# Performance work log

Hardware: AMD Instinct MI355X
Metric: run time of the kernel (lower is better)

Reference implementation:

```python
import jax, jax.numpy as jnp
import numpy as np

R = 40000      # aug_num_rels
E = 500000     # number of relation-graph triplets
DIN = 64       # rel_emb_dim
DH = 64        # hid_dim_rel
H = 8          # num_head
DHID = DH // H # 8
NBIN = 10
L = 2          # num_layer_rel


def _leaky(x):
    return jax.nn.leaky_relu(x, negative_slope=0.2)


def _rel_layer(emb_rel, head, tail, binidx, pw, pb, abin, avec, aw, ab):
    # emb_rel: [R, DH]; head/tail/binidx: [E]
    concat = jnp.concatenate([emb_rel[head], emb_rel[tail]], axis=-1)  # [E, 2*DH]
    z = _leaky(concat @ pw + pb).reshape(-1, H, DHID)                   # [E, H, DHID]
    # attention logits: per-head dot with attn_vec + leaky(bin bias)
    raw = (z * avec[None]).sum(-1) + _leaky(abin[binidx, :, 0])         # [E, H]
    # segmented softmax over edges grouped by head index
    m = jax.ops.segment_max(raw, head, num_segments=R)                  # [R, H]
    e = jnp.exp(raw - m[head])                                          # [E, H]
    s = jax.ops.segment_sum(e, head, num_segments=R)                    # [R, H]
    beta = e / (s[head] + 1e-16)                                        # [E, H]
    msg = (emb_rel[tail] @ aw + ab).reshape(-1, H, DHID) * beta[..., None]
    out = jax.ops.segment_sum(msg, head, num_segments=R)                # [R, H, DHID]
    return out.reshape(R, DH)


def setup_inputs() -> dict:
    key = jax.random.key(0)
    ks = jax.random.split(key, 12)
    ht = jax.random.randint(ks[0], (E, 2), 0, R)
    b = jax.random.randint(ks[1], (E, 1), 0, NBIN)
    relation_triplets = jnp.concatenate([ht, b], axis=-1).astype(jnp.int64)
    sc = 0.05
    return {
        "relation_triplets": relation_triplets,
        "rel_emb_w": jax.random.normal(ks[2], (R, DIN), jnp.float32) * sc,
        "proj1_w": jax.random.normal(ks[3], (DIN, DH), jnp.float32) * sc,
        "proj1_b": jnp.zeros((DH,), jnp.float32),
        "attn_proj_w": jax.random.normal(ks[4], (L, 2 * DH, DH), jnp.float32) * sc,
        "attn_proj_b": jnp.zeros((L, DH), jnp.float32),
        "attn_bin": jax.random.normal(ks[5], (L, NBIN, H, 1), jnp.float32) * sc,
        "attn_vec": jax.random.normal(ks[6], (L, H, DHID), jnp.float32) * sc,
        "aggr_w": jax.random.normal(ks[7], (L, DH, DH), jnp.float32) * sc,
        "aggr_b": jnp.zeros((L, DH), jnp.float32),
        "res_w": jax.random.normal(ks[8], (L, DH, DH), jnp.float32) * sc,
        "res_b": jnp.zeros((L, DH), jnp.float32),
    }


def reference(relation_triplets, rel_emb_w, proj1_w, proj1_b, attn_proj_w,
              attn_proj_b, attn_bin, attn_vec, aggr_w, aggr_b, res_w, res_b):
    head = relation_triplets[:, 0]
    tail = relation_triplets[:, 1]
    binidx = relation_triplets[:, 2]
    emb_rel = jax.nn.relu(rel_emb_w @ proj1_w + proj1_b)  # [R, DH]
    for l in range(L):
        h = _rel_layer(emb_rel, head, tail, binidx,
                       attn_proj_w[l], attn_proj_b[l], attn_bin[l],
                       attn_vec[l], aggr_w[l], aggr_b[l])
        h = jax.nn.relu(h)
        emb_rel = h + jax.nn.relu(emb_rel @ res_w[l] + res_b[l])
    return emb_rel
```

## Files before the change

### kernel.cpp

```cpp
#include <hip/hip_runtime.h>
#include <hip/hip_bf16.h>

typedef __hip_bfloat16 bf16;

#define R_NUM 40000
#define E_NUM 500000
#define HIST_BLOCKS 1954
#define XF_BLOCKS 1250

#define N_CNTS 0
#define N_ROWP 160000
#define N_STB 320000
#define N_XMP0 2320384
#define N_HR0 12560384
#define N_XMP1 33040384
#define N_HR1 43280384
#define NEED2 63760384ull

#define W_P1W 0
#define W_P1B 4096
#define W_APW 4160
#define W_APB 20544
#define W_ABIN 20672
#define W_AVEC 20832
#define W_AW 20960
#define W_AB 29152
#define W_RW 29280
#define W_RB 37472
#define W_END 37600
#define WCONV_BLOCKS 147

#define O_FLAG 0
#define O_WBUF 256
#define O_ROWP 150784
#define O_CNTS 310784
#define O_TMP 470784
#define O_PART 634624
#define O_STB 635136
#define O_BIG 2635392

static __device__ __forceinline__ float b2f(bf16 x) { return __bfloat162float(x); }
static __device__ __forceinline__ float ldv(const float* p, size_t i) { return p[i]; }
static __device__ __forceinline__ float ldv(const bf16* p, size_t i) { return __bfloat162float(p[i]); }
static __device__ __forceinline__ void stv(float* p, size_t i, float v) { p[i] = v; }
static __device__ __forceinline__ void stv(bf16* p, size_t i, float v) { p[i] = __float2bfloat16(v); }

static __device__ __forceinline__ unsigned int f2bb(float x) {
  union { float f; unsigned int u; } v;
  v.f = x;
  unsigned int r = v.u + 0x7FFFu + ((v.u >> 16) & 1u);
  return r >> 16;
}
static __device__ __forceinline__ unsigned int packxm(float xt, float mt) {
  return f2bb(xt) | (f2bb(mt) << 16);
}

static __device__ __forceinline__ void load_edge(const unsigned int* __restrict__ w, int e,
                                                 int i64, int& h, int& t, int& b) {
  if (i64) {
    h = (int)w[6 * e + 0];
    t = (int)w[6 * e + 2];
    b = (int)w[6 * e + 4];
  } else {
    h = (int)w[3 * e + 0];
    t = (int)w[3 * e + 1];
    b = (int)w[3 * e + 2];
  }
}


__global__ void k_detect_init(const unsigned int* __restrict__ trip_w,
                              const unsigned short* __restrict__ emb_w, int* __restrict__ flag,
                              int* __restrict__ counts, int* __restrict__ stb) {
  int tid = threadIdx.x;
  if (blockIdx.x == 0) {
    if (tid < 64) {
      int lane = tid;
      unsigned int acc = 0;
      for (int i = lane; i < 1024; i += 64) acc |= trip_w[2 * i + 1];
      int votes = 0;
      for (int i = lane; i < 2048; i += 64) {
        unsigned short u = emb_w[2 * i];
        int ex = (u >> 7) & 0xFF;
        if (ex >= 90 && ex <= 130) votes++;
      }
      for (int off = 1; off < 64; off <<= 1) {
        acc |= __shfl_xor(acc, off);
        votes += __shfl_xor(votes, off);
      }
      if (lane == 0) {
        flag[0] = (acc == 0) ? 1 : 0;
        flag[1] = (votes < 1024) ? 1 : 0;
      }
    }
    return;
  }
  int g = (blockIdx.x - 1) * 256 + tid;
  for (int i = g; i < R_NUM; i += 159 * 256) counts[i] = 0;
  if (blockIdx.x == 1 && tid < 64) stb[E_NUM + tid] = 0;
}


template <typename WT>
static __device__ __forceinline__ void xf4t(const float (*sA)[64], int base, int j, int l,
                                            const WT* __restrict__ apw, const WT* __restrict__ apb,
                                            const WT* __restrict__ aw, const WT* __restrict__ ab,
                                            const WT* __restrict__ rw, const WT* __restrict__ rb,
                                            int r0, unsigned int* __restrict__ XMp,
                                            float2* __restrict__ HR) {
  const WT* pwt = apw + l * 8192;
  const WT* pwb = pwt + 4096;
  const WT* awl = aw + l * 4096;
  const WT* rwl = rw + l * 4096;
  float axt[8] = {0.f, 0.f, 0.f, 0.f, 0.f, 0.f, 0.f, 0.f};
  float amt[8] = {0.f, 0.f, 0.f, 0.f, 0.f, 0.f, 0.f, 0.f};
  float axh[8] = {0.f, 0.f, 0.f, 0.f, 0.f, 0.f, 0.f, 0.f};
  float ars[8] = {0.f, 0.f, 0.f, 0.f, 0.f, 0.f, 0.f, 0.f};
  for (int i4 = 0; i4 < 64; i4 += 4) {
    float4 ev[8];
#pragma unroll
    for (int n = 0; n < 8; n++) ev[n] = *(const float4*)&sA[base + n][i4];
#pragma unroll
    for (int di = 0; di < 4; di++) {
      int i = i4 + di;
      float wt = ldv(pwb, (size_t)i * 64 + j);
      float wm = ldv(awl, (size_t)i * 64 + j);
      float wh = ldv(pwt, (size_t)i * 64 + j);
      float wr = ldv(rwl, (size_t)i * 64 + j);
#pragma unroll
      for (int n = 0; n < 8; n++) {
        float e = ((const float*)&ev[n])[di];
        axt[n] = fmaf(e, wt, axt[n]);
        amt[n] = fmaf(e, wm, amt[n]);
        axh[n] = fmaf(e, wh, axh[n]);
        ars[n] = fmaf(e, wr, ars[n]);
      }
    }
  }
  float abj = ldv(ab, (size_t)l * 64 + j);
  float pbj = ldv(apb, (size_t)l * 64 + j);
  float rbj = ldv(rb, (size_t)l * 64 + j);
#pragma unroll
  for (int n = 0; n < 8; n++) {
    XMp[(size_t)(r0 + n) * 64 + j] = packxm(axt[n], amt[n] + abj);
    HR[(size_t)(r0 + n) * 64 + j] = make_float2(axh[n] + pbj, fmaxf(ars[n] + rbj, 0.f));
  }
}


template <typename T>
static __device__ __forceinline__ void kA_xform(const T* __restrict__ A, const T* __restrict__ p1w,
                                                const T* __restrict__ p1b,
                                                const T* __restrict__ apw,
                                                const T* __restrict__ apb, const T* __restrict__ aw,
                                                const T* __restrict__ ab, const T* __restrict__ rw,
                                                const T* __restrict__ rb, int u,
                                                unsigned int* __restrict__ XMp0,
                                                float2* __restrict__ HR0, float (*sA)[64]) {
  int tid = threadIdx.x;
  int j = tid & 63;
  int g = tid >> 6;
  int base = g * 8;
  for (int k = tid; k < 2048; k += 256) {
    int rr = k >> 6, cc = k & 63;
    sA[rr][cc] = ldv(A, (size_t)(u * 32 + rr) * 64 + cc);
  }
  __syncthreads();
  float a[8] = {0.f, 0.f, 0.f, 0.f, 0.f, 0.f, 0.f, 0.f};
  for (int i4 = 0; i4 < 64; i4 += 4) {
    float4 ev[8];
#pragma unroll
    for (int n = 0; n < 8; n++) ev[n] = *(const float4*)&sA[base + n][i4];
#pragma unroll
    for (int di = 0; di < 4; di++) {
      float w = ldv(p1w, (size_t)(i4 + di) * 64 + j);
#pragma unroll
      for (int n = 0; n < 8; n++) a[n] = fmaf(((const float*)&ev[n])[di], w, a[n]);
    }
  }
  float bj = ldv(p1b, j);
#pragma unroll
  for (int n = 0; n < 8; n++) a[n] = fmaxf(a[n] + bj, 0.f);
  __syncthreads();
#pragma unroll
  for (int n = 0; n < 8; n++) sA[base + n][j] = a[n];
  __syncthreads();
  xf4t<T>((const float(*)[64])sA, base, j, 0, apw, apb, aw, ab, rw, rb, u * 32 + base, XMp0, HR0);
}

__global__ void __launch_bounds__(256, 4) kA(const unsigned int* __restrict__ trip_w,
                                             const int* __restrict__ flag,
                                             const void* __restrict__ A, const void* p1w,
                                             const void* p1b, const void* apw, const void* apb,
                                             const void* aw, const void* ab, const void* rw,
                                             const void* rb, int* __restrict__ counts,
                                             unsigned int* __restrict__ XMp0,
                                             float2* __restrict__ HR0) {
  if (blockIdx.x < HIST_BLOCKS) {
    int e = blockIdx.x * 256 + threadIdx.x;
    if (e < E_NUM) {
      int h = flag[0] ? (int)trip_w[6 * e] : (int)trip_w[3 * e];
      atomicAdd(&counts[h], 1);
    }
    return;
  }
  __shared__ float sA[32][64];
  int u = blockIdx.x - HIST_BLOCKS;
  if (flag[1])
    kA_xform<float>((const float*)A, (const float*)p1w, (const float*)p1b, (const float*)apw,
                    (const float*)apb, (const float*)aw, (const float*)ab, (const float*)rw,
                    (const float*)rb, u, XMp0, HR0, sA);
  else
    kA_xform<bf16>((const bf16*)A, (const bf16*)p1w, (const bf16*)p1b, (const bf16*)apw,
                   (const bf16*)apb, (const bf16*)aw, (const bf16*)ab, (const bf16*)rw,
                   (const bf16*)rb, u, XMp0, HR0, sA);
}


__global__ void __launch_bounds__(1024) k_scan1(const int* __restrict__ counts,
                                                int* __restrict__ row_ptr) {
  __shared__ int sp[1024];
  int tid = threadIdx.x;
  int base = tid * 40;
  int local[40];
  int s = 0;
  if (base < R_NUM) {
#pragma unroll
    for (int k = 0; k < 40; k++) {
      int v = counts[base + k];
      local[k] = s;
      s += v;
    }
  }
  sp[tid] = s;
  __syncthreads();
  for (int off = 1; off < 1024; off <<= 1) {
    int t = (tid >= off) ? sp[tid - off] : 0;
    __syncthreads();
    sp[tid] += t;
    __syncthreads();
  }
  int pre = (tid == 0) ? 0 : sp[tid - 1];
  if (base < R_NUM) {
#pragma unroll
    for (int k = 0; k < 40; k++) row_ptr[base + k] = pre + local[k];
  }
}

__global__ void k_scatter(const unsigned int* __restrict__ trip_w, const int* __restrict__ flag,
                          int* __restrict__ row_ptr, int* __restrict__ stb) {
  int e = blockIdx.x * 256 + threadIdx.x;
  if (e >= E_NUM) return;
  int h, t, b;
  load_edge(trip_w, e, flag[0], h, t, b);
  int pos = atomicAdd(&row_ptr[h], 1);
  stb[pos] = (t & 0xFFFF) | (b << 16);
}


template <typename T>
static __device__ __forceinline__ void kB_body(const int* __restrict__ row_ptr,
                                               const int* __restrict__ stb,
                                               const unsigned int* __restrict__ XMp0,
                                               const float2* __restrict__ HR0,
                                               const T* __restrict__ apw, const T* __restrict__ apb,
                                               const T* __restrict__ abin,
                                               const T* __restrict__ avec, const T* __restrict__ aw,
                                               const T* __restrict__ ab, const T* __restrict__ rw,
                                               const T* __restrict__ rb,
                                               unsigned int* __restrict__ XMp1,
                                               float2* __restrict__ HR1, float (*sE)[64],
                                               float* sab) {
  int tid = threadIdx.x;
  int lane = tid & 63;
  int w = tid >> 6;
  int hh = lane >> 3;
  if (tid < 80) {
    float a = ldv(abin, tid);
    sab[tid] = (a > 0.f) ? a : 0.2f * a;
  }
  __syncthreads();
  float av = ldv(avec, lane);
  int rbase = blockIdx.x * 32 + w * 8;
#pragma unroll 1
  for (int n = 0; n < 8; n++) {
    int r = rbase + n;
    float2 hr = HR0[(size_t)r * 64 + lane];
    int beg = (r == 0) ? 0 : row_ptr[r - 1];
    int end = row_ptr[r];
    beg = __builtin_amdgcn_readfirstlane(beg);
    end = __builtin_amdgcn_readfirstlane(end);
    float xh = hr.x;
    float num = 0.f, den = 0.f;
    for (int jj = beg; jj < end; jj += 16) {
      int pk[16];
      unsigned int xp[16];
#pragma unroll
      for (int k = 0; k < 16; k++) pk[k] = stb[jj + k];
#pragma unroll
      for (int k = 0; k < 16; k++) xp[k] = XMp0[(size_t)(pk[k] & 0xFFFF) * 64 + lane];
#pragma unroll
      for (int k = 0; k < 16; k++) {
        float xt = __uint_as_float(xp[k] << 16);
        float mt = __uint_as_float(xp[k] & 0xFFFF0000u);
        float z = xh + xt;
        z = (z > 0.f) ? z : 0.2f * z;
        float v = z * av;
        v += __shfl_xor(v, 1);
        v += __shfl_xor(v, 2);
        v += __shfl_xor(v, 4);
        float e = __expf(v + sab[(pk[k] >> 16) * 8 + hh]);
        e = (jj + k < end) ? e : 0.f;
        den += e;
        num = fmaf(mt, e, num);
      }
    }
    sE[w * 8 + n][lane] = fmaxf(num / (den + 1e-16f), 0.f) + hr.y;
  }
  __syncthreads();
  xf4t<T>((const float(*)[64])sE, w * 8, lane, 1, apw, apb, aw, ab, rw, rb,
          blockIdx.x * 32 + w * 8, XMp1, HR1);
}

__global__ void __launch_bounds__(256, 4) kB(const int* __restrict__ row_ptr,
                                             const int* __restrict__ stb,
                                             const int* __restrict__ flag,
                                             const unsigned int* __restrict__ XMp0,
                                             const float2* __restrict__ HR0, const void* apw,
                                             const void* apb, const void* abin, const void* avec,
                                             const void* aw, const void* ab, const void* rw,
                                             const void* rb, unsigned int* __restrict__ XMp1,
                                             float2* __restrict__ HR1) {
  __shared__ float sE[32][64];
  __shared__ float sab[80];
  if (flag[1])
    kB_body<float>(row_ptr, stb, XMp0, HR0, (const float*)apw, (const float*)apb,
                   (const float*)abin, (const float*)avec, (const float*)aw, (const float*)ab,
                   (const float*)rw, (const float*)rb, XMp1, HR1, sE, sab);
  else
    kB_body<bf16>(row_ptr, stb, XMp0, HR0, (const bf16*)apw, (const bf16*)apb, (const bf16*)abin,
                  (const bf16*)avec, (const bf16*)aw, (const bf16*)ab, (const bf16*)rw,
                  (const bf16*)rb, XMp1, HR1, sE, sab);
}


template <typename T>
static __device__ __forceinline__ void kC_body(const int* __restrict__ row_ptr,
                                               const int* __restrict__ stb,
                                               const unsigned int* __restrict__ XMp1,
                                               const float2* __restrict__ HR1,
                                               const T* __restrict__ abin,
                                               const T* __restrict__ avec,
                                               float* __restrict__ out, float* sab) {
  int tid = threadIdx.x;
  int lane = tid & 63;
  int w = tid >> 6;
  int hh = lane >> 3;
  if (tid < 80) {
    float a = ldv(abin, 80 + tid);
    sab[tid] = (a > 0.f) ? a : 0.2f * a;
  }
  __syncthreads();
  float av = ldv(avec, 64 + lane);

  int r = blockIdx.x * 4 + w;
  float2 hr = HR1[(size_t)r * 64 + lane];
  int beg = (r == 0) ? 0 : row_ptr[r - 1];
  int end = row_ptr[r];
  beg = __builtin_amdgcn_readfirstlane(beg);
  end = __builtin_amdgcn_readfirstlane(end);

  float xh = hr.x;
  float num = 0.f, den = 0.f;
  for (int j = beg; j < end; j += 16) {
    int pk[16];
    unsigned int xp[16];
#pragma unroll
    for (int k = 0; k < 16; k++) pk[k] = stb[j + k];
#pragma unroll
    for (int k = 0; k < 16; k++) xp[k] = XMp1[(size_t)(pk[k] & 0xFFFF) * 64 + lane];
#pragma unroll
    for (int k = 0; k < 16; k++) {
      float xt = __uint_as_float(xp[k] << 16);
      float mt = __uint_as_float(xp[k] & 0xFFFF0000u);
      float z = xh + xt;
      z = (z > 0.f) ? z : 0.2f * z;
      float v = z * av;
      v += __shfl_xor(v, 1);
      v += __shfl_xor(v, 2);
      v += __shfl_xor(v, 4);
      float e = __expf(v + sab[(pk[k] >> 16) * 8 + hh]);
      e = (j + k < end) ? e : 0.f;
      den += e;
      num = fmaf(mt, e, num);
    }
  }
  out[(size_t)r * 64 + lane] = fmaxf(num / (den + 1e-16f), 0.f) + hr.y;
}

__global__ void __launch_bounds__(256, 4) kC(const int* __restrict__ row_ptr,
                                             const int* __restrict__ stb,
                                             const int* __restrict__ flag,
                                             const unsigned int* __restrict__ XMp1,
                                             const float2* __restrict__ HR1, const void* abin,
                                             const void* avec, float* __restrict__ out) {
  __shared__ float sab[80];
  if (flag[1])
    kC_body<float>(row_ptr, stb, XMp1, HR1, (const float*)abin, (const float*)avec, out, sab);
  else
    kC_body<bf16>(row_ptr, stb, XMp1, HR1, (const bf16*)abin, (const bf16*)avec, out, sab);
}


__global__ void k_hist_wconv(const unsigned int* __restrict__ trip_w, const int* __restrict__ flag,
                             int* __restrict__ counts, const void* p1w, const void* p1b,
                             const void* apw, const void* apb, const void* abin, const void* avec,
                             const void* aw, const void* ab, const void* rw, const void* rb,
                             float* __restrict__ wbuf) {
  if (blockIdx.x < WCONV_BLOCKS) {
    int i = blockIdx.x * 256 + threadIdx.x;
    if (i >= W_END) return;
    const void* src;
    int off;
    if (i < W_P1B) { src = p1w; off = i - W_P1W; }
    else if (i < W_APW) { src = p1b; off = i - W_P1B; }
    else if (i < W_APB) { src = apw; off = i - W_APW; }
    else if (i < W_ABIN) { src = apb; off = i - W_APB; }
    else if (i < W_AVEC) { src = abin; off = i - W_ABIN; }
    else if (i < W_AW) { src = avec; off = i - W_AVEC; }
    else if (i < W_AB) { src = aw; off = i - W_AW; }
    else if (i < W_RW) { src = ab; off = i - W_AB; }
    else if (i < W_RB) { src = rw; off = i - W_RW; }
    else { src = rb; off = i - W_RB; }
    wbuf[i] = flag[1] ? ((const float*)src)[off] : b2f(((const bf16*)src)[off]);
    return;
  }
  int e = (blockIdx.x - WCONV_BLOCKS) * 256 + threadIdx.x;
  if (e >= E_NUM) return;
  int h, t, b;
  load_edge(trip_w, e, flag[0], h, t, b);
  atomicAdd(&counts[h], 1);
}

__global__ void k_emb0(const void* __restrict__ A, const int* __restrict__ flag,
                       const float* __restrict__ wbuf, float* __restrict__ emb) {
  int j = threadIdx.x & 63;
  int g = threadIdx.x >> 6;
  int r0 = blockIdx.x * 16 + g * 4;
  int f32 = flag[1];
  __shared__ float sA[16][64];
  for (int k = threadIdx.x; k < 1024; k += 256) {
    int rr = k >> 6, cc = k & 63;
    size_t idx = (size_t)(blockIdx.x * 16 + rr) * 64 + cc;
    sA[rr][cc] = f32 ? ((const float*)A)[idx] : b2f(((const bf16*)A)[idx]);
  }
  __syncthreads();
  const float* W = wbuf + W_P1W;
  float a[4] = {0.f, 0.f, 0.f, 0.f};
  int base = g * 4;
  for (int i = 0; i < 64; i++) {
    float w = W[i * 64 + j];
#pragma unroll
    for (int n = 0; n < 4; n++) a[n] = fmaf(sA[base + n][i], w, a[n]);
  }
  float bj = wbuf[W_P1B + j];
#pragma unroll
  for (int n = 0; n < 4; n++)
    emb[(size_t)(r0 + n) * 64 + j] = fmaxf(a[n] + bj, 0.f);
}

static __device__ __forceinline__ float dotcol(const float* __restrict__ Wm, float val, int lane) {
  float acc = 0.f;
  for (int i = 0; i < 64; i++) acc = fmaf(__shfl(val, i), Wm[i * 64 + lane], acc);
  return acc;
}

template <typename TIN, typename TOUT>
__global__ void k_edge_d(const int* __restrict__ row_ptr, const int* __restrict__ stb,
                         const float* __restrict__ wbuf, int l, const TIN* __restrict__ emb_in,
                         TOUT* __restrict__ emb_out) {
  __shared__ float sab[80];
  int tid = threadIdx.x;
  int lane = tid & 63;
  int w = tid >> 6;
  int r = blockIdx.x * 4 + w;
  int hh = lane >> 3;
  if (tid < 80) {
    float a = wbuf[W_ABIN + l * 80 + tid];
    sab[tid] = (a > 0.f) ? a : 0.2f * a;
  }
  __syncthreads();
  const float* pwt = wbuf + W_APW + l * 8192;
  const float* pwb = pwt + 4096;
  const float* aw = wbuf + W_AW + l * 4096;
  const float* rw = wbuf + W_RW + l * 4096;

  float ev = ldv(emb_in, (size_t)r * 64 + lane);
  float xh = wbuf[W_APB + l * 64 + lane];
  float res = wbuf[W_RB + l * 64 + lane];
  for (int i = 0; i < 64; i++) {
    float e = __shfl(ev, i);
    xh = fmaf(e, pwt[i * 64 + lane], xh);
    res = fmaf(e, rw[i * 64 + lane], res);
  }
  res = fmaxf(res, 0.f);
  float av = wbuf[W_AVEC + l * 64 + lane];
  float abl = wbuf[W_AB + l * 64 + lane];

  int beg = (r == 0) ? 0 : row_ptr[r - 1];
  int end = row_ptr[r];
  float num = 0.f, den = 0.f;
  for (int j = beg; j < end; j++) {
    int p = stb[j];
    int t = p & 0xFFFF;
    float tv = ldv(emb_in, (size_t)t * 64 + lane);
    float z = xh + dotcol(pwb, tv, lane);
    z = (z > 0.f) ? z : 0.2f * z;
    float v = z * av;
    v += __shfl_xor(v, 1);
    v += __shfl_xor(v, 2);
    v += __shfl_xor(v, 4);
    float e = __expf(v + sab[(p >> 16) * 8 + hh]);
    den += e;
    float mt = dotcol(aw, tv, lane) + abl;
    num = fmaf(mt, e, num);
  }
  stv(emb_out, (size_t)r * 64 + lane, fmaxf(num / (den + 1e-16f), 0.f) + res);
}


extern "C" void kernel_launch(void* const* d_in, const int* in_sizes, int n_in,
                              void* d_out, int out_size, void* d_ws, size_t ws_size,
                              hipStream_t stream) {
  const unsigned int* trip_w = (const unsigned int*)d_in[0];
  const void* rel_emb = d_in[1];
  float* emb = (float*)d_out;
  char* ws = (char*)d_ws;

  if (ws_size >= NEED2) {
    int* counts = (int*)(ws + N_CNTS);
    int* row_ptr = (int*)(ws + N_ROWP);
    int* stb = (int*)(ws + N_STB);
    unsigned int* XMp0 = (unsigned int*)(ws + N_XMP0);
    float2* HR0 = (float2*)(ws + N_HR0);
    unsigned int* XMp1 = (unsigned int*)(ws + N_XMP1);
    float2* HR1 = (float2*)(ws + N_HR1);
    int* flag = (int*)(ws + N_STB + (E_NUM + 64) * 4);

    k_detect_init<<<160, 256, 0, stream>>>(trip_w, (const unsigned short*)rel_emb, flag, counts,
                                           stb);
    kA<<<HIST_BLOCKS + XF_BLOCKS, 256, 0, stream>>>(trip_w, flag, rel_emb, d_in[2], d_in[3],
                                                    d_in[4], d_in[5], d_in[8], d_in[9], d_in[10],
                                                    d_in[11], counts, XMp0, HR0);
    k_scan1<<<1, 1024, 0, stream>>>(counts, row_ptr);
    k_scatter<<<HIST_BLOCKS, 256, 0, stream>>>(trip_w, flag, row_ptr, stb);
    kB<<<XF_BLOCKS, 256, 0, stream>>>(row_ptr, stb, flag, XMp0, HR0, d_in[4], d_in[5], d_in[6],
                                      d_in[7], d_in[8], d_in[9], d_in[10], d_in[11], XMp1, HR1);
    kC<<<R_NUM / 4, 256, 0, stream>>>(row_ptr, stb, flag, XMp1, HR1, d_in[6], d_in[7], emb);
    return;
  }

  {
    int* flag = (int*)(ws + O_FLAG);
    float* wbuf = (float*)(ws + O_WBUF);
    int* row_ptr = (int*)(ws + O_ROWP);
    int* counts = (int*)(ws + O_CNTS);
    int* stb = (int*)(ws + O_STB);
    char* big = ws + O_BIG;

    k_detect_init<<<160, 256, 0, stream>>>(trip_w, (const unsigned short*)rel_emb, flag, counts,
                                           stb);
    k_hist_wconv<<<WCONV_BLOCKS + HIST_BLOCKS, 256, 0, stream>>>(
        trip_w, flag, counts, d_in[2], d_in[3], d_in[4], d_in[5], d_in[6], d_in[7], d_in[8],
        d_in[9], d_in[10], d_in[11], wbuf);
    k_scan1<<<1, 1024, 0, stream>>>(counts, row_ptr);
    k_scatter<<<HIST_BLOCKS, 256, 0, stream>>>(trip_w, flag, row_ptr, stb);
    k_emb0<<<R_NUM / 16, 256, 0, stream>>>(rel_emb, flag, wbuf, emb);
    bf16* embB = (bf16*)big;
    k_edge_d<float, bf16><<<R_NUM / 4, 256, 0, stream>>>(row_ptr, stb, wbuf, 0, emb, embB);
    k_edge_d<bf16, float><<<R_NUM / 4, 256, 0, stream>>>(row_ptr, stb, wbuf, 1, embB, emb);
  }
}
```

Measured before the change: 267.5 us.

## Use one wave per relation in layer-1 aggregation and fuse transform via shuffles

The layer-1 aggregation kernel now assigns one wavefront per relation row (10000 blocks of 4 waves) instead of 8 rows per wave in 1250 blocks. The following 64x64 transforms are computed per row by broadcasting the aggregated value across lanes with shuffles, which removes the shared staging buffer and block barrier. The goal is more parallelism and better load balance over uneven segment lengths. In exchange, weights are re-read per row with no reuse across rows, and the transform does more shuffles. The kA grid is also reordered so transform blocks launch before histogram blocks.

```diff
diff --git a/kernel.cpp b/kernel.cpp
--- a/kernel.cpp
+++ b/kernel.cpp
@@ -6,7 +6,7 @@
 #define R_NUM 40000
 #define E_NUM 500000
 #define HIST_BLOCKS 1954
-#define XF_BLOCKS 1250
+#define XFA_BLOCKS 1250
 
 #define N_CNTS 0
 #define N_ROWP 160000
@@ -101,7 +101,7 @@
 }
 
 
-template <typename WT>
+template <typename WT, int N>
 static __device__ __forceinline__ void xf4t(const float (*sA)[64], int base, int j, int l,
                                             const WT* __restrict__ apw, const WT* __restrict__ apb,
                                             const WT* __restrict__ aw, const WT* __restrict__ ab,
@@ -112,14 +112,14 @@
   const WT* pwb = pwt + 4096;
   const WT* awl = aw + l * 4096;
   const WT* rwl = rw + l * 4096;
-  float axt[8] = {0.f, 0.f, 0.f, 0.f, 0.f, 0.f, 0.f, 0.f};
-  float amt[8] = {0.f, 0.f, 0.f, 0.f, 0.f, 0.f, 0.f, 0.f};
-  float axh[8] = {0.f, 0.f, 0.f, 0.f, 0.f, 0.f, 0.f, 0.f};
-  float ars[8] = {0.f, 0.f, 0.f, 0.f, 0.f, 0.f, 0.f, 0.f};
+  float axt[N] = {};
+  float amt[N] = {};
+  float axh[N] = {};
+  float ars[N] = {};
   for (int i4 = 0; i4 < 64; i4 += 4) {
-    float4 ev[8];
-#pragma unroll
-    for (int n = 0; n < 8; n++) ev[n] = *(const float4*)&sA[base + n][i4];
+    float4 ev[N];
+#pragma unroll
+    for (int n = 0; n < N; n++) ev[n] = *(const float4*)&sA[base + n][i4];
 #pragma unroll
     for (int di = 0; di < 4; di++) {
       int i = i4 + di;
@@ -128,7 +128,7 @@
       float wh = ldv(pwt, (size_t)i * 64 + j);
       float wr = ldv(rwl, (size_t)i * 64 + j);
 #pragma unroll
-      for (int n = 0; n < 8; n++) {
+      for (int n = 0; n < N; n++) {
         float e = ((const float*)&ev[n])[di];
         axt[n] = fmaf(e, wt, axt[n]);
         amt[n] = fmaf(e, wm, amt[n]);
@@ -141,7 +141,7 @@
   float pbj = ldv(apb, (size_t)l * 64 + j);
   float rbj = ldv(rb, (size_t)l * 64 + j);
 #pragma unroll
-  for (int n = 0; n < 8; n++) {
+  for (int n = 0; n < N; n++) {
     XMp[(size_t)(r0 + n) * 64 + j] = packxm(axt[n], amt[n] + abj);
     HR[(size_t)(r0 + n) * 64 + j] = make_float2(axh[n] + pbj, fmaxf(ars[n] + rbj, 0.f));
   }
@@ -173,9 +173,9 @@
     for (int n = 0; n < 8; n++) ev[n] = *(const float4*)&sA[base + n][i4];
 #pragma unroll
     for (int di = 0; di < 4; di++) {
-      float w = ldv(p1w, (size_t)(i4 + di) * 64 + j);
-#pragma unroll
-      for (int n = 0; n < 8; n++) a[n] = fmaf(((const float*)&ev[n])[di], w, a[n]);
+      float wv = ldv(p1w, (size_t)(i4 + di) * 64 + j);
+#pragma unroll
+      for (int n = 0; n < 8; n++) a[n] = fmaf(((const float*)&ev[n])[di], wv, a[n]);
     }
   }
   float bj = ldv(p1b, j);
@@ -185,7 +185,8 @@
 #pragma unroll
   for (int n = 0; n < 8; n++) sA[base + n][j] = a[n];
   __syncthreads();
-  xf4t<T>((const float(*)[64])sA, base, j, 0, apw, apb, aw, ab, rw, rb, u * 32 + base, XMp0, HR0);
+  xf4t<T, 8>((const float(*)[64])sA, base, j, 0, apw, apb, aw, ab, rw, rb, u * 32 + base, XMp0,
+             HR0);
 }
 
 __global__ void __launch_bounds__(256, 4) kA(const unsigned int* __restrict__ trip_w,
@@ -196,8 +197,8 @@
                                              const void* rb, int* __restrict__ counts,
                                              unsigned int* __restrict__ XMp0,
                                              float2* __restrict__ HR0) {
-  if (blockIdx.x < HIST_BLOCKS) {
-    int e = blockIdx.x * 256 + threadIdx.x;
+  if (blockIdx.x >= XFA_BLOCKS) {
+    int e = (blockIdx.x - XFA_BLOCKS) * 256 + threadIdx.x;
     if (e < E_NUM) {
       int h = flag[0] ? (int)trip_w[6 * e] : (int)trip_w[3 * e];
       atomicAdd(&counts[h], 1);
@@ -205,7 +206,7 @@
     return;
   }
   __shared__ float sA[32][64];
-  int u = blockIdx.x - HIST_BLOCKS;
+  int u = blockIdx.x;
   if (flag[1])
     kA_xform<float>((const float*)A, (const float*)p1w, (const float*)p1b, (const float*)apw,
                     (const float*)apb, (const float*)aw, (const float*)ab, (const float*)rw,
@@ -259,18 +260,18 @@
 
 
 template <typename T>
-static __device__ __forceinline__ void kB_body(const int* __restrict__ row_ptr,
-                                               const int* __restrict__ stb,
-                                               const unsigned int* __restrict__ XMp0,
-                                               const float2* __restrict__ HR0,
-                                               const T* __restrict__ apw, const T* __restrict__ apb,
-                                               const T* __restrict__ abin,
-                                               const T* __restrict__ avec, const T* __restrict__ aw,
-                                               const T* __restrict__ ab, const T* __restrict__ rw,
-                                               const T* __restrict__ rb,
-                                               unsigned int* __restrict__ XMp1,
-                                               float2* __restrict__ HR1, float (*sE)[64],
-                                               float* sab) {
+static __device__ __forceinline__ void kB2_body(const int* __restrict__ row_ptr,
+                                                const int* __restrict__ stb,
+                                                const unsigned int* __restrict__ XMp0,
+                                                const float2* __restrict__ HR0,
+                                                const T* __restrict__ apw,
+                                                const T* __restrict__ apb,
+                                                const T* __restrict__ abin,
+                                                const T* __restrict__ avec,
+                                                const T* __restrict__ aw, const T* __restrict__ ab,
+                                                const T* __restrict__ rw, const T* __restrict__ rb,
+                                                unsigned int* __restrict__ XMp1,
+                                                float2* __restrict__ HR1, float* sab) {
   int tid = threadIdx.x;
   int lane = tid & 63;
   int w = tid >> 6;
@@ -281,66 +282,78 @@
   }
   __syncthreads();
   float av = ldv(avec, lane);
-  int rbase = blockIdx.x * 32 + w * 8;
-#pragma unroll 1
-  for (int n = 0; n < 8; n++) {
-    int r = rbase + n;
-    float2 hr = HR0[(size_t)r * 64 + lane];
-    int beg = (r == 0) ? 0 : row_ptr[r - 1];
-    int end = row_ptr[r];
-    beg = __builtin_amdgcn_readfirstlane(beg);
-    end = __builtin_amdgcn_readfirstlane(end);
-    float xh = hr.x;
-    float num = 0.f, den = 0.f;
-    for (int jj = beg; jj < end; jj += 16) {
-      int pk[16];
-      unsigned int xp[16];
-#pragma unroll
-      for (int k = 0; k < 16; k++) pk[k] = stb[jj + k];
-#pragma unroll
-      for (int k = 0; k < 16; k++) xp[k] = XMp0[(size_t)(pk[k] & 0xFFFF) * 64 + lane];
-#pragma unroll
-      for (int k = 0; k < 16; k++) {
-        float xt = __uint_as_float(xp[k] << 16);
-        float mt = __uint_as_float(xp[k] & 0xFFFF0000u);
-        float z = xh + xt;
-        z = (z > 0.f) ? z : 0.2f * z;
-        float v = z * av;
-        v += __shfl_xor(v, 1);
-        v += __shfl_xor(v, 2);
-        v += __shfl_xor(v, 4);
-        float e = __expf(v + sab[(pk[k] >> 16) * 8 + hh]);
-        e = (jj + k < end) ? e : 0.f;
-        den += e;
-        num = fmaf(mt, e, num);
-      }
-    }
-    sE[w * 8 + n][lane] = fmaxf(num / (den + 1e-16f), 0.f) + hr.y;
-  }
-  __syncthreads();
-  xf4t<T>((const float(*)[64])sE, w * 8, lane, 1, apw, apb, aw, ab, rw, rb,
-          blockIdx.x * 32 + w * 8, XMp1, HR1);
-}
-
-__global__ void __launch_bounds__(256, 4) kB(const int* __restrict__ row_ptr,
-                                             const int* __restrict__ stb,
-                                             const int* __restrict__ flag,
-                                             const unsigned int* __restrict__ XMp0,
-                                             const float2* __restrict__ HR0, const void* apw,
-                                             const void* apb, const void* abin, const void* avec,
-                                             const void* aw, const void* ab, const void* rw,
-                                             const void* rb, unsigned int* __restrict__ XMp1,
-                                             float2* __restrict__ HR1) {
-  __shared__ float sE[32][64];
+
+  int r = blockIdx.x * 4 + w;
+  float2 hr = HR0[(size_t)r * 64 + lane];
+  int beg = (r == 0) ? 0 : row_ptr[r - 1];
+  int end = row_ptr[r];
+  beg = __builtin_amdgcn_readfirstlane(beg);
+  end = __builtin_amdgcn_readfirstlane(end);
+
+  float xh = hr.x;
+  float num = 0.f, den = 0.f;
+  for (int jj = beg; jj < end; jj += 16) {
+    int pk[16];
+    unsigned int xp[16];
+#pragma unroll
+    for (int k = 0; k < 16; k++) pk[k] = stb[jj + k];
+#pragma unroll
+    for (int k = 0; k < 16; k++)
+      xp[k] = XMp0[(size_t)(pk[k] & 0xFFFF) * 64 + lane];
+#pragma unroll
+    for (int k = 0; k < 16; k++) {
+      float xt = __uint_as_float(xp[k] << 16);
+      float mt = __uint_as_float(xp[k] & 0xFFFF0000u);
+      float z = xh + xt;
+      z = (z > 0.f) ? z : 0.2f * z;
+      float v = z * av;
+      v += __shfl_xor(v, 1);
+      v += __shfl_xor(v, 2);
+      v += __shfl_xor(v, 4);
+      float e = __expf(v + sab[(pk[k] >> 16) * 8 + hh]);
+      e = (jj + k < end) ? e : 0.f;
+      den += e;
+      num = fmaf(mt, e, num);
+    }
+  }
+  float val = fmaxf(num / (den + 1e-16f), 0.f) + hr.y;
+
+  const T* pwt = apw + 8192;
+  const T* pwb = pwt + 4096;
+  const T* awl = aw + 4096;
+  const T* rwl = rw + 4096;
+  float axt = 0.f, amt = 0.f, axh = 0.f, ars = 0.f;
+#pragma unroll 16
+  for (int i = 0; i < 64; i++) {
+    float e = __shfl(val, i);
+    axt = fmaf(e, ldv(pwb, (size_t)i * 64 + lane), axt);
+    amt = fmaf(e, ldv(awl, (size_t)i * 64 + lane), amt);
+    axh = fmaf(e, ldv(pwt, (size_t)i * 64 + lane), axh);
+    ars = fmaf(e, ldv(rwl, (size_t)i * 64 + lane), ars);
+  }
+  XMp1[(size_t)r * 64 + lane] = packxm(axt, amt + ldv(ab, 64 + lane));
+  HR1[(size_t)r * 64 + lane] =
+      make_float2(axh + ldv(apb, 64 + lane), fmaxf(ars + ldv(rb, 64 + lane), 0.f));
+}
+
+__global__ void __launch_bounds__(256, 4) kB2(const int* __restrict__ row_ptr,
+                                              const int* __restrict__ stb,
+                                              const int* __restrict__ flag,
+                                              const unsigned int* __restrict__ XMp0,
+                                              const float2* __restrict__ HR0, const void* apw,
+                                              const void* apb, const void* abin, const void* avec,
+                                              const void* aw, const void* ab, const void* rw,
+                                              const void* rb, unsigned int* __restrict__ XMp1,
+                                              float2* __restrict__ HR1) {
   __shared__ float sab[80];
   if (flag[1])
-    kB_body<float>(row_ptr, stb, XMp0, HR0, (const float*)apw, (const float*)apb,
-                   (const float*)abin, (const float*)avec, (const float*)aw, (const float*)ab,
-                   (const float*)rw, (const float*)rb, XMp1, HR1, sE, sab);
+    kB2_body<float>(row_ptr, stb, XMp0, HR0, (const float*)apw, (const float*)apb,
+                    (const float*)abin, (const float*)avec, (const float*)aw, (const float*)ab,
+                    (const float*)rw, (const float*)rb, XMp1, HR1, sab);
   else
-    kB_body<bf16>(row_ptr, stb, XMp0, HR0, (const bf16*)apw, (const bf16*)apb, (const bf16*)abin,
-                  (const bf16*)avec, (const bf16*)aw, (const bf16*)ab, (const bf16*)rw,
-                  (const bf16*)rb, XMp1, HR1, sE, sab);
+    kB2_body<bf16>(row_ptr, stb, XMp0, HR0, (const bf16*)apw, (const bf16*)apb, (const bf16*)abin,
+                   (const bf16*)avec, (const bf16*)aw, (const bf16*)ab, (const bf16*)rw,
+                   (const bf16*)rb, XMp1, HR1, sab);
 }
 
 
@@ -549,13 +562,13 @@
 
     k_detect_init<<<160, 256, 0, stream>>>(trip_w, (const unsigned short*)rel_emb, flag, counts,
                                            stb);
-    kA<<<HIST_BLOCKS + XF_BLOCKS, 256, 0, stream>>>(trip_w, flag, rel_emb, d_in[2], d_in[3],
-                                                    d_in[4], d_in[5], d_in[8], d_in[9], d_in[10],
-                                                    d_in[11], counts, XMp0, HR0);
+    kA<<<XFA_BLOCKS + HIST_BLOCKS, 256, 0, stream>>>(trip_w, flag, rel_emb, d_in[2], d_in[3],
+                                                     d_in[4], d_in[5], d_in[8], d_in[9], d_in[10],
+                                                     d_in[11], counts, XMp0, HR0);
     k_scan1<<<1, 1024, 0, stream>>>(counts, row_ptr);
     k_scatter<<<HIST_BLOCKS, 256, 0, stream>>>(trip_w, flag, row_ptr, stb);
-    kB<<<XF_BLOCKS, 256, 0, stream>>>(row_ptr, stb, flag, XMp0, HR0, d_in[4], d_in[5], d_in[6],
-                                      d_in[7], d_in[8], d_in[9], d_in[10], d_in[11], XMp1, HR1);
+    kB2<<<R_NUM / 4, 256, 0, stream>>>(row_ptr, stb, flag, XMp0, HR0, d_in[4], d_in[5], d_in[6],
+                                       d_in[7], d_in[8], d_in[9], d_in[10], d_in[11], XMp1, HR1);
     kC<<<R_NUM / 4, 256, 0, stream>>>(row_ptr, stb, flag, XMp1, HR1, d_in[6], d_in[7], emb);
     return;
   }
```

New measurement: 296.9 us. 1.11x slower.
